# Optimization experiments

Hardware: AMD Instinct MI355X
Metric: run time of the kernel (lower is better)

## Reference

```python
import jax, jax.numpy as jnp
import numpy as np

B, P, H, W = 64, 50000, 512, 512


def setup_inputs() -> dict:
    key = jax.random.key(0)
    ks = jax.random.split(key, 6)
    x = jax.random.normal(ks[0], (B, 1, H, W), dtype=jnp.float32)
    x_A = jax.random.randint(ks[1], (B, P), 0, W, dtype=jnp.int32)
    y_A = jax.random.randint(ks[2], (B, P), 0, H, dtype=jnp.int32)
    x_B = jax.random.randint(ks[3], (B, P), 0, W, dtype=jnp.int32)
    y_B = jax.random.randint(ks[4], (B, P), 0, H, dtype=jnp.int32)
    # ordinal relation in {-1, 0, 1}: -1/+1 = ordered pair, 0 = equal depth
    gt = jax.random.randint(ks[5], (B, P), -1, 2).astype(jnp.float32)
    return {"x": x, "x_A": x_A, "y_A": y_A, "x_B": x_B, "y_B": y_B, "gt": gt}


def reference(x, x_A, y_A, x_B, y_B, gt):
    # x: [B,1,H,W] predicted depth; gather z values at sparse point pairs.
    img = x[:, 0]                              # [B,H,W]
    b = jnp.arange(B)[:, None]                 # [B,1] batch index for gather
    z_A = img[b, y_A, x_A]                     # [B,P]
    z_B = img[b, y_B, x_B]                     # [B,P]
    d = z_A - z_B
    mask = jnp.abs(gt)                         # 1 for ordered pairs, 0 for equal
    # ranking loss log(1+exp(-gt*d)) for ordered pairs, (d)^2 for equal pairs
    loss = mask * jnp.log1p(jnp.exp(-gt * d)) + (1.0 - mask) * d * d
    n_point_total = B * P
    return jnp.sum(loss) / n_point_total
```

## Files before the change

### kernel.cpp

```cpp
#include <hip/hip_runtime.h>

#define THREADS 256

__global__ __launch_bounds__(THREADS) void rdc_kernel(
    const float* __restrict__ x,
    const int*   __restrict__ xA,
    const int*   __restrict__ yA,
    const int*   __restrict__ xB,
    const int*   __restrict__ yB,
    const float* __restrict__ gt,
    float* __restrict__ out,
    int nvec, float inv_n)
{
    const int P4 = 50000 / 4;
    const int HW = 512 * 512;

    float acc = 0.0f;
    const int stride = gridDim.x * blockDim.x;
    for (int v = blockIdx.x * blockDim.x + threadIdx.x; v < nvec; v += stride) {
        const int4  xa = reinterpret_cast<const int4*>(xA)[v];
        const int4  ya = reinterpret_cast<const int4*>(yA)[v];
        const int4  xb = reinterpret_cast<const int4*>(xB)[v];
        const int4  yb = reinterpret_cast<const int4*>(yB)[v];
        const float4 g = reinterpret_cast<const float4*>(gt)[v];

        const int b = v / P4;
        const float* __restrict__ img = x + (size_t)b * HW;

        #pragma unroll
        for (int j = 0; j < 4; ++j) {
            int xai = (j == 0) ? xa.x : (j == 1) ? xa.y : (j == 2) ? xa.z : xa.w;
            int yai = (j == 0) ? ya.x : (j == 1) ? ya.y : (j == 2) ? ya.z : ya.w;
            int xbi = (j == 0) ? xb.x : (j == 1) ? xb.y : (j == 2) ? xb.z : xb.w;
            int ybi = (j == 0) ? yb.x : (j == 1) ? yb.y : (j == 2) ? yb.z : yb.w;
            float gi = (j == 0) ? g.x  : (j == 1) ? g.y  : (j == 2) ? g.z  : g.w;

            float zA = img[(yai << 9) + xai];
            float zB = img[(ybi << 9) + xbi];
            float d  = zA - zB;

            float t  = -gi * d;
            float sp = fmaxf(t, 0.0f) + log1pf(__expf(-fabsf(t)));
            float m  = fabsf(gi);
            acc += m * sp + (1.0f - m) * d * d;
        }
    }

    #pragma unroll
    for (int off = 32; off > 0; off >>= 1)
        acc += __shfl_down(acc, off, 64);

    __shared__ float wsum[THREADS / 64];
    const int lane = threadIdx.x & 63;
    const int wid  = threadIdx.x >> 6;
    if (lane == 0) wsum[wid] = acc;
    __syncthreads();
    if (threadIdx.x == 0) {
        float s = 0.0f;
        #pragma unroll
        for (int i = 0; i < THREADS / 64; ++i) s += wsum[i];
        atomicAdd(out, s * inv_n);
    }
}

extern "C" void kernel_launch(void* const* d_in, const int* in_sizes, int n_in,
                              void* d_out, int out_size, void* d_ws, size_t ws_size,
                              hipStream_t stream) {
    const float* x  = (const float*)d_in[0];
    const int*   xA = (const int*)d_in[1];
    const int*   yA = (const int*)d_in[2];
    const int*   xB = (const int*)d_in[3];
    const int*   yB = (const int*)d_in[4];
    const float* gt = (const float*)d_in[5];
    float* out = (float*)d_out;

    const int n    = in_sizes[1];
    const int nvec = n / 4;
    const float inv_n = 1.0f / (float)n;

    hipMemsetAsync(out, 0, sizeof(float), stream);

    const int blocks = (nvec + THREADS - 1) / THREADS;
    rdc_kernel<<<blocks, THREADS, 0, stream>>>(x, xA, yA, xB, yB, gt, out, nvec, inv_n);
}
```

Baseline: 195.5 us.

## Pin batch images to XCDs and stream index arrays with nontemporal loads

Launches a fixed grid of 192 blocks per XCD, assuming round-robin block placement, and assigns each XCD eight contiguous batch images, so each XCD's L2 only serves gathers from its own 8 MB of image data rather than all 64 MB. Index and label arrays are read with nontemporal loads so this streaming data does not evict image lines. The cost is hard-coded B/P/XCD constants and reliance on the hardware's block-to-XCD mapping; the grid-stride loop becomes persistent.

```diff
diff --git a/kernel.cpp b/kernel.cpp
--- a/kernel.cpp
+++ b/kernel.cpp
@@ -1,6 +1,12 @@
 #include <hip/hip_runtime.h>
 
 #define THREADS 256
+#define BLOCKS_PER_XCD 192
+#define NXCD 8
+#define NBLOCKS (BLOCKS_PER_XCD * NXCD)
+
+typedef int   intx4   __attribute__((ext_vector_type(4)));
+typedef float floatx4 __attribute__((ext_vector_type(4)));
 
 __global__ __launch_bounds__(THREADS) void rdc_kernel(
     const float* __restrict__ x,
@@ -10,34 +16,39 @@
     const int*   __restrict__ yB,
     const float* __restrict__ gt,
     float* __restrict__ out,
-    int nvec, float inv_n)
+    float inv_n)
 {
-    const int P4 = 50000 / 4;
-    const int HW = 512 * 512;
+    const int P4  = 12500;
+    const int BPX = 8;
+    const int HW  = 512 * 512;
+
+    const int xcd = blockIdx.x & 7;
+    const int lb  = blockIdx.x >> 3;
+    const int tlocal = lb * THREADS + threadIdx.x;
+    const int nthreads_xcd = BLOCKS_PER_XCD * THREADS;
+    const int total = BPX * P4;
 
     float acc = 0.0f;
-    const int stride = gridDim.x * blockDim.x;
-    for (int v = blockIdx.x * blockDim.x + threadIdx.x; v < nvec; v += stride) {
-        const int4  xa = reinterpret_cast<const int4*>(xA)[v];
-        const int4  ya = reinterpret_cast<const int4*>(yA)[v];
-        const int4  xb = reinterpret_cast<const int4*>(xB)[v];
-        const int4  yb = reinterpret_cast<const int4*>(yB)[v];
-        const float4 g = reinterpret_cast<const float4*>(gt)[v];
+    for (int j = tlocal; j < total; j += nthreads_xcd) {
+        const int bl = j / P4;
+        const int i  = j - bl * P4;
+        const int b  = xcd * BPX + bl;
+        const int v  = b * P4 + i;
 
-        const int b = v / P4;
+        const intx4  xa = __builtin_nontemporal_load((const intx4*)xA + v);
+        const intx4  ya = __builtin_nontemporal_load((const intx4*)yA + v);
+        const intx4  xb = __builtin_nontemporal_load((const intx4*)xB + v);
+        const intx4  yb = __builtin_nontemporal_load((const intx4*)yB + v);
+        const floatx4 g = __builtin_nontemporal_load((const floatx4*)gt + v);
+
         const float* __restrict__ img = x + (size_t)b * HW;
 
         #pragma unroll
-        for (int j = 0; j < 4; ++j) {
-            int xai = (j == 0) ? xa.x : (j == 1) ? xa.y : (j == 2) ? xa.z : xa.w;
-            int yai = (j == 0) ? ya.x : (j == 1) ? ya.y : (j == 2) ? ya.z : ya.w;
-            int xbi = (j == 0) ? xb.x : (j == 1) ? xb.y : (j == 2) ? xb.z : xb.w;
-            int ybi = (j == 0) ? yb.x : (j == 1) ? yb.y : (j == 2) ? yb.z : yb.w;
-            float gi = (j == 0) ? g.x  : (j == 1) ? g.y  : (j == 2) ? g.z  : g.w;
-
-            float zA = img[(yai << 9) + xai];
-            float zB = img[(ybi << 9) + xbi];
+        for (int k = 0; k < 4; ++k) {
+            float zA = img[(ya[k] << 9) + xa[k]];
+            float zB = img[(yb[k] << 9) + xb[k]];
             float d  = zA - zB;
+            float gi = g[k];
 
             float t  = -gi * d;
             float sp = fmaxf(t, 0.0f) + log1pf(__expf(-fabsf(t)));
@@ -58,7 +69,7 @@
     if (threadIdx.x == 0) {
         float s = 0.0f;
         #pragma unroll
-        for (int i = 0; i < THREADS / 64; ++i) s += wsum[i];
+        for (int i2 = 0; i2 < THREADS / 64; ++i2) s += wsum[i2];
         atomicAdd(out, s * inv_n);
     }
 }
@@ -74,12 +85,9 @@
     const float* gt = (const float*)d_in[5];
     float* out = (float*)d_out;
 
-    const int n    = in_sizes[1];
-    const int nvec = n / 4;
+    const int n = in_sizes[1];
     const float inv_n = 1.0f / (float)n;
 
     hipMemsetAsync(out, 0, sizeof(float), stream);
-
-    const int blocks = (nvec + THREADS - 1) / THREADS;
-    rdc_kernel<<<blocks, THREADS, 0, stream>>>(x, xA, yA, xB, yB, gt, out, nvec, inv_n);
+    rdc_kernel<<<NBLOCKS, THREADS, 0, stream>>>(x, xA, yA, xB, yB, gt, out, inv_n);
 }
```

Measured after the change: 170.0 us. 1.15x faster.
